# Kernel tuning notes

Hardware: AMD Instinct MI355X
Metric: run time of the kernel (lower is better)

The kernel has to match this reference:

```python
import jax, jax.numpy as jnp
import numpy as np

NHEAD = 3
NPTS = 5
HID = 96
B_GRAPHS = 16384
COORDS_WEIGHT = 1.0


def _ln(x, g, b):
    mu = jnp.mean(x, -1, keepdims=True)
    v = jnp.mean((x - mu) ** 2, -1, keepdims=True)
    return (x - mu) / jnp.sqrt(v + 1e-5) * g + b


def _build_edge_index():
    # fully-connected per graph, grouped by source node (row-major over sources)
    idx = np.arange(NPTS)
    src = np.repeat(idx, NPTS - 1)
    dst = np.concatenate([np.delete(idx, i) for i in range(NPTS)])
    off = (np.arange(B_GRAPHS) * NPTS)[:, None]
    row = (off + src[None, :]).reshape(-1)
    col = (off + dst[None, :]).reshape(-1)
    return jnp.asarray(np.stack([row, col]), dtype=jnp.int32)


def setup_inputs():
    key = jax.random.key(0)
    ks = jax.random.split(key, 24)
    Nn = B_GRAPHS * NPTS          # 81920 nodes
    E = B_GRAPHS * NPTS * (NPTS - 1)  # 327680 edges

    def w(k, i, o):
        return jax.random.normal(k, (i, o), jnp.float32) * (1.0 / np.sqrt(i))

    inp = {
        'h': jax.random.normal(ks[0], (Nn, HID), jnp.float32),
        'edge_index': _build_edge_index(),
        'coord': jax.random.normal(ks[1], (Nn, 3), jnp.float32),
        'coord_pre': jax.random.normal(ks[2], (Nn, 3), jnp.float32),
        'vel': jax.random.normal(ks[3], (Nn, 3), jnp.float32),
        'edge_attr': jax.random.normal(ks[4], (E, HID), jnp.float32),
        # edge_mlp
        'ew1': w(ks[5], 3 * HID, HID), 'eb1': jnp.zeros((HID,), jnp.float32),
        'ew2': w(ks[6], HID, HID), 'eb2': jnp.zeros((HID,), jnp.float32),
        # edge_mlp_enhance
        'xw1': w(ks[7], 3 * HID, HID), 'xb1': jnp.zeros((HID,), jnp.float32),
        'xw2': w(ks[8], HID, HID), 'xb2': jnp.zeros((HID,), jnp.float32),
        # node_mlp
        'nw1': w(ks[9], 2 * HID, HID), 'nb1': jnp.zeros((HID,), jnp.float32),
        'nw2': w(ks[10], HID, HID), 'nb2': jnp.zeros((HID,), jnp.float32),
        # coord_mlp_inner
        'cw1': w(ks[11], HID, HID), 'cb1': jnp.zeros((HID,), jnp.float32),
        'cw2': w(ks[12], HID, HID), 'cb2': jnp.zeros((HID,), jnp.float32),
        'cw3': w(ks[13], HID, 3), 'cb3': jnp.zeros((3,), jnp.float32),
        # attention projections
        'qw': w(ks[14], HID, HID), 'qb': jnp.zeros((HID,), jnp.float32),
        'kw': w(ks[15], 2 * HID, HID), 'kb': jnp.zeros((HID,), jnp.float32),
        'vw': w(ks[16], HID, HID), 'vb': jnp.zeros((HID,), jnp.float32),
        # layernorms
        'g1': jnp.ones((HID,), jnp.float32), 'be1': jnp.zeros((HID,), jnp.float32),
        'g2': jnp.ones((HID,), jnp.float32), 'be2': jnp.zeros((HID,), jnp.float32),
    }
    return inp


def _forward(h, edge_index, coord, coord_pre, vel, edge_attr,
             ew1, eb1, ew2, eb2, xw1, xb1, xw2, xb2, nw1, nb1, nw2, nb2,
             cw1, cb1, cw2, cb2, cw3, cb3, qw, qb, kw, kb, vw, vb,
             g1, be1, g2, be2):
    sp = jax.nn.softplus
    row, col = edge_index[0], edge_index[1]
    n_nodes = h.shape[0]

    # edge_model (attention flag is False)
    ef = sp(jnp.concatenate([h[row], h[col], edge_attr], 1) @ ew1 + eb1)
    ef = sp(ef @ ew2 + eb2)  # [E, C]

    B, N, C = n_nodes // NPTS, NPTS, ef.shape[-1]
    d = C // NHEAD
    q = h.reshape(B, N, C)
    m = ef.reshape(B, N, N - 1, C)
    h_m = jnp.concatenate(
        [jnp.broadcast_to(q[:, :, None, :], (B, N, N - 1, C)), m], -1
    ).reshape(B, N * (N - 1), 2 * C)

    qh = (q @ qw + qb).reshape(B, N, NHEAD, d).transpose(0, 2, 1, 3)           # [B,H,N,d]
    kh = (h_m @ kw + kb).reshape(B, N * (N - 1), NHEAD, d).transpose(0, 2, 1, 3)
    kh = kh.reshape(B, NHEAD, N, N - 1, d)                                      # [B,H,N,N-1,d]
    vh = (ef.reshape(B, N * (N - 1), C) @ vw + vb).reshape(B, N * (N - 1), NHEAD, d).transpose(0, 2, 1, 3)

    scores = jnp.einsum('bhnd,bhnkd->bhnk', qh, kh) / jnp.sqrt(jnp.float32(d))
    attw = jax.nn.softmax(scores, -1)                                           # [B,H,N,N-1]
    m_update = attw.reshape(B, NHEAD, N * (N - 1), 1) * vh                      # [B,H,E',d]
    att_edge_feat = m_update.transpose(0, 2, 1, 3).reshape(-1, C)               # [E, C]

    # node_model
    agg = jax.ops.segment_sum(att_edge_feat, row, num_segments=n_nodes)
    agg = _ln(agg, g1, be1)
    out = sp(jnp.concatenate([h, agg], 1) @ nw1 + nb1) @ nw2 + nb2
    hn = _ln(h + out, g2, be2)

    # edge enhance
    ef2 = ef + (sp(jnp.concatenate([hn[row], hn[col], edge_attr], 1) @ xw1 + xb1) @ xw2 + xb2)

    # coord2radial on coord_pre (norm_diff=False)
    cd = coord_pre[row] - coord_pre[col]
    cc = jnp.cross(coord_pre[row], coord_pre[col])
    cv = jnp.cross(cd, cc)

    # acc_model_inner
    t = sp(ef2 @ cw1 + cb1)
    t = sp(t @ cw2 + cb2)
    bc = t @ cw3 + cb3                                                          # [E, 3]
    trans = jnp.clip(cd * bc[:, :1] + cc * bc[:, 1:2] + cv * bc[:, 2:3], -100.0, 100.0)
    s = jax.ops.segment_sum(trans, row, num_segments=n_nodes)
    cnt = jax.ops.segment_sum(jnp.ones_like(trans), row, num_segments=n_nodes)
    acc = (s / jnp.maximum(cnt, 1.0)) * COORDS_WEIGHT

    return acc, hn, ef2


def reference(h, edge_index, coord, coord_pre, vel, edge_attr,
              ew1, eb1, ew2, eb2, xw1, xb1, xw2, xb2, nw1, nb1, nw2, nb2,
              cw1, cb1, cw2, cb2, cw3, cb3, qw, qb, kw, kb, vw, vb,
              g1, be1, g2, be2):
    return _forward(h, edge_index, coord, coord_pre, vel, edge_attr,
                    ew1, eb1, ew2, eb2, xw1, xb1, xw2, xb2, nw1, nb1, nw2, nb2,
                    cw1, cb1, cw2, cb2, cw3, cb3, qw, qb, kw, kb, vw, vb,
                    g1, be1, g2, be2)
```

## Files before the change

kernel.cpp:

```cpp
#include <hip/hip_runtime.h>
#include <hip/hip_bf16.h>

#define B_GRAPHS 16384
#define NN (B_GRAPHS * 5)
#define NE (NN * 4)
#define GPB 4
#define EPB 80
#define NPB 20

typedef __attribute__((ext_vector_type(8))) short bf8;
typedef __attribute__((ext_vector_type(4))) short s4;
typedef __attribute__((ext_vector_type(4))) float f4;
typedef __attribute__((ext_vector_type(2))) unsigned u2;
typedef __attribute__((ext_vector_type(4))) unsigned u4;

#define OFF_EW1 0
#define OFF_EW2 27648
#define OFF_KW  36864
#define OFF_VW  55296
#define OFF_QW  64512
#define OFF_NW1 73728
#define OFF_NW2 92160
#define OFF_XW1 101376
#define OFF_XW2 129024
#define OFF_CW1 138240
#define OFF_CW2 147456

__device__ __forceinline__ float sp_f(float x) {
    return fmaxf(x, 0.0f) + __logf(1.0f + __expf(-fabsf(x)));
}
__device__ __forceinline__ short tobf(float x) {
    return __builtin_bit_cast(short, __float2bfloat16(x));
}
__device__ __forceinline__ float frombf(short s) {
    union { float f; unsigned u; } v;
    v.u = ((unsigned)(unsigned short)s) << 16;
    return v.f;
}
__device__ __forceinline__ unsigned pk2(float a, float b) {
    unsigned lo = (unsigned short)tobf(a);
    unsigned hi = (unsigned short)tobf(b);
    return lo | (hi << 16);
}
__device__ __forceinline__ bf8 ldfrag(const short* buf, int row, int k) {
    return *(const bf8*)&buf[(row * 96 + k) ^ ((row & 7) << 3)];
}
__device__ __forceinline__ void stpk(short* buf, int row, int col0, f4 v) {
    u2 o = {pk2(v[0], v[1]), pk2(v[2], v[3])};
    *(u2*)&buf[(row * 96 + col0) ^ ((row & 7) << 3)] = o;
}
__device__ __forceinline__ void stpk8(short* buf, int row, int col0,
                                      const float* v) {
    u4 o = {pk2(v[0], v[1]), pk2(v[2], v[3]), pk2(v[4], v[5]), pk2(v[6], v[7])};
    *(u4*)&buf[(row * 96 + col0) ^ ((row & 7) << 3)] = o;
}

template <int K, int NS, class AF>
__device__ __forceinline__ void gemmCol(const short* __restrict__ wT, int wc0,
                                        int ln, int kg, AF aload, f4* acc) {
    constexpr int NK = K / 32;
    bf8 wf[NK];
    const short* wp = wT + (size_t)(wc0 + ln) * K + kg * 8;
#pragma unroll
    for (int kk = 0; kk < NK; kk++) wf[kk] = *(const bf8*)(wp + kk * 32);
#pragma unroll
    for (int s = 0; s < NS; s++) {
        acc[s][0] = 0.f; acc[s][1] = 0.f; acc[s][2] = 0.f; acc[s][3] = 0.f;
    }
#pragma unroll
    for (int kk = 0; kk < NK; kk++) {
#pragma unroll
        for (int s = 0; s < NS; s++) {
            acc[s] = __builtin_amdgcn_mfma_f32_16x16x32_bf16(wf[kk],
                                                             aload(s, kk * 32),
                                                             acc[s], 0, 0, 0);
        }
    }
}

__global__ __launch_bounds__(256) void k_prep(
    const float* ew1, const float* ew2, const float* kw, const float* vw,
    const float* qw, const float* nw1, const float* nw2, const float* xw1,
    const float* xw2, const float* cw1, const float* cw2, short* wsT) {
    const float* srcs[11] = {ew1, ew2, kw, vw, qw, nw1, nw2, xw1, xw2, cw1, cw2};
    const int Ks[11] = {288, 96, 192, 96, 96, 192, 96, 288, 96, 96, 96};
    const int offs[11] = {OFF_EW1, OFF_EW2, OFF_KW, OFF_VW, OFF_QW, OFF_NW1,
                          OFF_NW2, OFF_XW1, OFF_XW2, OFF_CW1, OFF_CW2};
    int b = blockIdx.x;
    const float* src = srcs[b];
    int K = Ks[b], off = offs[b];
    for (int idx = threadIdx.x; idx < K * 96; idx += 256) {
        int n = idx / K, k = idx - n * K;
        wsT[off + idx] = tobf(src[(size_t)k * 96 + n]);
    }
}

__global__ __launch_bounds__(384, 4) void k_fused(
    const float* __restrict__ h, const float* __restrict__ cp,
    const float* __restrict__ ea, const short* __restrict__ wsT,
    const float* __restrict__ eb1, const float* __restrict__ eb2,
    const float* __restrict__ qb, const float* __restrict__ kb,
    const float* __restrict__ vb, const float* __restrict__ nb1,
    const float* __restrict__ nb2, const float* __restrict__ g1,
    const float* __restrict__ be1, const float* __restrict__ g2,
    const float* __restrict__ be2, const float* __restrict__ xb1,
    const float* __restrict__ xb2, const float* __restrict__ cb1,
    const float* __restrict__ cb2, const float* __restrict__ cw3,
    const float* __restrict__ cb3,
    float* __restrict__ accg, float* __restrict__ hng, float* __restrict__ efg) {
    __shared__ __align__(16) short smem[19680];
    short* hb = smem;
    short* SB = smem + 1920;
    short* E1 = smem + 3840;
    short* E2 = smem + 11520;
    float* sc   = (float*)(smem + 19200);
    float* bcb  = sc;
    float* cw3s = (float*)SB;
    float* trs  = (float*)(SB + 640);

    const int t = threadIdx.x;
    const int blk = blockIdx.x;
    const int n0 = blk * NPB, e0 = blk * EPB;

    for (int i = t; i < 1920; i += 384) {
        int r = i / 24, c = (i - r * 24) * 4;
        f4 v = *(const f4*)&ea[(size_t)(e0 + r) * 96 + c];
        stpk(E2, r, c, v);
    }
    for (int i = t; i < 480; i += 384) {
        int r = i / 24, c = (i - r * 24) * 4;
        f4 v = *(const f4*)&h[(size_t)(n0 + r) * 96 + c];
        stpk(hb, r, c, v);
    }
    __syncthreads();

    const int lane = t & 63, w = t >> 6;
    const int kg = lane >> 4, ln = lane & 15;
    const int wc0 = w * 16, col0 = wc0 + kg * 4;

    int erow[5], esrc[5], edst[5];
#pragma unroll
    for (int s = 0; s < 5; s++) {
        erow[s] = s * 16 + ln;
        int sl = erow[s] >> 2;
        esrc[s] = sl;
        int si = sl % 5, jj = erow[s] & 3;
        edst[s] = (sl / 5) * 5 + jj + (jj >= si);
    }

    f4 acc[5];
    gemmCol<288, 5>(wsT + OFF_EW1, wc0, ln, kg,
        [&](int s, int k0) -> bf8 {
            int k = k0 + kg * 8;
            if (k0 < 96)  return ldfrag(hb, esrc[s], k);
            if (k0 < 192) return ldfrag(hb, edst[s], k - 96);
            return ldfrag(E2, erow[s], k - 192);
        }, acc);
    {
        f4 b = *(const f4*)&eb1[col0];
#pragma unroll
        for (int s = 0; s < 5; s++) {
            f4 v;
#pragma unroll
            for (int j = 0; j < 4; j++) v[j] = sp_f(acc[s][j] + b[j]);
            stpk(E1, erow[s], col0, v);
        }
    }
    __syncthreads();
    gemmCol<96, 5>(wsT + OFF_EW2, wc0, ln, kg,
        [&](int s, int k0) { return ldfrag(E1, erow[s], k0 + kg * 8); }, acc);
    {
        f4 qa[2];
        gemmCol<96, 2>(wsT + OFF_QW, wc0, ln, kg,
            [&](int s, int k0) { return ldfrag(hb, s * 16 + ln, k0 + kg * 8); }, qa);
        f4 b = *(const f4*)&eb2[col0];
#pragma unroll
        for (int s = 0; s < 5; s++) {
            f4 v;
#pragma unroll
            for (int j = 0; j < 4; j++) v[j] = sp_f(acc[s][j] + b[j]);
            stpk(E2, erow[s], col0, v);
        }
        f4 bq = *(const f4*)&qb[col0];
#pragma unroll
        for (int s = 0; s < 2; s++) {
            int row = s * 16 + ln;
            if (row < NPB) {
                f4 v;
#pragma unroll
                for (int j = 0; j < 4; j++) v[j] = qa[s][j] + bq[j];
                stpk(SB, row, col0, v);
            }
        }
    }
    __syncthreads();
    gemmCol<192, 5>(wsT + OFF_KW, wc0, ln, kg,
        [&](int s, int k0) {
            int k = k0 + kg * 8;
            if (k0 < 96) return ldfrag(hb, esrc[s], k);
            return ldfrag(E2, erow[s], k - 96);
        }, acc);
    {
        f4 b = *(const f4*)&kb[col0];
#pragma unroll
        for (int s = 0; s < 5; s++) {
            f4 v;
#pragma unroll
            for (int j = 0; j < 4; j++) v[j] = acc[s][j] + b[j];
            stpk(E1, erow[s], col0, v);
        }
    }
    __syncthreads();
    if (t < 240) {
        int e = t / 3, hd = t - e * 3, nd = e >> 2;
        float s = 0.f;
#pragma unroll
        for (int c8 = 0; c8 < 4; c8++) {
            int c = hd * 32 + c8 * 8;
            bf8 qv = ldfrag(SB, nd, c);
            bf8 kv = ldfrag(E1, e, c);
#pragma unroll
            for (int j = 0; j < 8; j++) s = fmaf(frombf(qv[j]), frombf(kv[j]), s);
        }
        sc[e * 3 + hd] = s * 0.17677669529663687f;
    }
    __syncthreads();
    if (t < 60) {
        int nd = t / 3, hd = t - nd * 3;
        float v0 = sc[(nd * 4 + 0) * 3 + hd], v1 = sc[(nd * 4 + 1) * 3 + hd];
        float v2 = sc[(nd * 4 + 2) * 3 + hd], v3 = sc[(nd * 4 + 3) * 3 + hd];
        float m = fmaxf(fmaxf(v0, v1), fmaxf(v2, v3));
        float p0 = __expf(v0 - m), p1 = __expf(v1 - m);
        float p2 = __expf(v2 - m), p3 = __expf(v3 - m);
        float inv = 1.f / (p0 + p1 + p2 + p3);
        sc[(nd * 4 + 0) * 3 + hd] = p0 * inv;
        sc[(nd * 4 + 1) * 3 + hd] = p1 * inv;
        sc[(nd * 4 + 2) * 3 + hd] = p2 * inv;
        sc[(nd * 4 + 3) * 3 + hd] = p3 * inv;
    }
    gemmCol<96, 5>(wsT + OFF_VW, wc0, ln, kg,
        [&](int s, int k0) { return ldfrag(E2, erow[s], k0 + kg * 8); }, acc);
    {
        f4 b = *(const f4*)&vb[col0];
#pragma unroll
        for (int s = 0; s < 5; s++) {
            f4 v;
#pragma unroll
            for (int j = 0; j < 4; j++) v[j] = acc[s][j] + b[j];
            stpk(E1, erow[s], col0, v);
        }
    }
    __syncthreads();
    if (t < 320) {
        int nd = t >> 4, cg = t & 15;
        bool act = cg < 12;
        int hd = cg >> 2;
        float agg[8];
#pragma unroll
        for (int j = 0; j < 8; j++) agg[j] = 0.f;
        if (act) {
#pragma unroll
            for (int k = 0; k < 4; k++) {
                int e = nd * 4 + k;
                float wgt = sc[e * 3 + hd];
                bf8 v8 = ldfrag(E1, e, cg * 8);
#pragma unroll
                for (int j = 0; j < 8; j++) agg[j] = fmaf(wgt, frombf(v8[j]), agg[j]);
            }
        }
        float s1 = 0.f, s2 = 0.f;
#pragma unroll
        for (int j = 0; j < 8; j++) { s1 += agg[j]; s2 += agg[j] * agg[j]; }
        if (!act) { s1 = 0.f; s2 = 0.f; }
        for (int m = 1; m < 16; m <<= 1) {
            s1 += __shfl_xor(s1, m);
            s2 += __shfl_xor(s2, m);
        }
        float mu = s1 * (1.f / 96.f);
        float var = s2 * (1.f / 96.f) - mu * mu;
        float rs = rsqrtf(var + 1e-5f);
        if (act) {
            int c = cg * 8;
            f4 ga = *(const f4*)&g1[c], gb = *(const f4*)&g1[c + 4];
            f4 ba = *(const f4*)&be1[c], bb = *(const f4*)&be1[c + 4];
            float o[8];
#pragma unroll
            for (int j = 0; j < 4; j++) {
                o[j] = (agg[j] - mu) * rs * ga[j] + ba[j];
                o[j + 4] = (agg[j + 4] - mu) * rs * gb[j] + bb[j];
            }
            stpk8(SB, nd, c, o);
        }
    }
    __syncthreads();
    {
        f4 eav[5];
        int rr[5], cc[5];
#pragma unroll
        for (int u = 0; u < 5; u++) {
            int i = t + u * 384;
            rr[u] = i / 24; cc[u] = (i - rr[u] * 24) * 4;
            eav[u] = *(const f4*)&ea[(size_t)(e0 + rr[u]) * 96 + cc[u]];
        }
        f4 na[2];
        gemmCol<192, 2>(wsT + OFF_NW1, wc0, ln, kg,
            [&](int s, int k0) {
                int row = s * 16 + ln, k = k0 + kg * 8;
                if (k0 < 96) return ldfrag(hb, row, k);
                return ldfrag(SB, row, k - 96);
            }, na);
        f4 b = *(const f4*)&nb1[col0];
        f4 t1v[2];
#pragma unroll
        for (int s = 0; s < 2; s++)
#pragma unroll
            for (int j = 0; j < 4; j++) t1v[s][j] = sp_f(na[s][j] + b[j]);
        __syncthreads();
#pragma unroll
        for (int s = 0; s < 2; s++) {
            int row = s * 16 + ln;
            if (row < NPB) stpk(SB, row, col0, t1v[s]);
        }
#pragma unroll
        for (int u = 0; u < 5; u++) stpk(E1, rr[u], cc[u], eav[u]);
    }
    __syncthreads();
    {
        f4 na[2];
        gemmCol<96, 2>(wsT + OFF_NW2, wc0, ln, kg,
            [&](int s, int k0) { return ldfrag(SB, s * 16 + ln, k0 + kg * 8); }, na);
        f4 b = *(const f4*)&nb2[col0];
#pragma unroll
        for (int s = 0; s < 2; s++) {
            int row = s * 16 + ln;
            if (row < NPB) {
                f4 hv = *(const f4*)&h[(size_t)(n0 + row) * 96 + col0];
                f4 v;
#pragma unroll
                for (int j = 0; j < 4; j++) v[j] = na[s][j] + b[j] + hv[j];
                stpk(hb, row, col0, v);
            }
        }
    }
    __syncthreads();
    if (t < 320) {
        int nd = t >> 4, cg = t & 15;
        bool act = cg < 12;
        float xv[8];
#pragma unroll
        for (int j = 0; j < 8; j++) xv[j] = 0.f;
        if (act) {
            bf8 x = ldfrag(hb, nd, cg * 8);
#pragma unroll
            for (int j = 0; j < 8; j++) xv[j] = frombf(x[j]);
        }
        float s1 = 0.f, s2 = 0.f;
#pragma unroll
        for (int j = 0; j < 8; j++) { s1 += xv[j]; s2 += xv[j] * xv[j]; }
        for (int m = 1; m < 16; m <<= 1) {
            s1 += __shfl_xor(s1, m);
            s2 += __shfl_xor(s2, m);
        }
        float mu = s1 * (1.f / 96.f);
        float var = s2 * (1.f / 96.f) - mu * mu;
        float rs = rsqrtf(var + 1e-5f);
        if (act) {
            int c = cg * 8;
            f4 ga = *(const f4*)&g2[c], gb = *(const f4*)&g2[c + 4];
            f4 ba = *(const f4*)&be2[c], bb = *(const f4*)&be2[c + 4];
            float o[8];
#pragma unroll
            for (int j = 0; j < 4; j++) {
                o[j] = (xv[j] - mu) * rs * ga[j] + ba[j];
                o[j + 4] = (xv[j + 4] - mu) * rs * gb[j] + bb[j];
            }
            f4 o0 = {o[0], o[1], o[2], o[3]}, o1 = {o[4], o[5], o[6], o[7]};
            *(f4*)&hng[(size_t)(n0 + nd) * 96 + c] = o0;
            *(f4*)&hng[(size_t)(n0 + nd) * 96 + c + 4] = o1;
            stpk8(hb, nd, c, o);
        }
    }
    __syncthreads();
    gemmCol<288, 5>(wsT + OFF_XW1, wc0, ln, kg,
        [&](int s, int k0) -> bf8 {
            int k = k0 + kg * 8;
            if (k0 < 96)  return ldfrag(hb, esrc[s], k);
            if (k0 < 192) return ldfrag(hb, edst[s], k - 96);
            return ldfrag(E1, erow[s], k - 192);
        }, acc);
    __syncthreads();
    {
        f4 b = *(const f4*)&xb1[col0];
#pragma unroll
        for (int s = 0; s < 5; s++) {
            f4 v;
#pragma unroll
            for (int j = 0; j < 4; j++) v[j] = sp_f(acc[s][j] + b[j]);
            stpk(E1, erow[s], col0, v);
        }
    }
    __syncthreads();
    gemmCol<96, 5>(wsT + OFF_XW2, wc0, ln, kg,
        [&](int s, int k0) { return ldfrag(E1, erow[s], k0 + kg * 8); }, acc);
    {
        f4 b = *(const f4*)&xb2[col0];
#pragma unroll
        for (int s = 0; s < 5; s++) {
            int row = erow[s];
            s4 ev = *(const s4*)&E2[(row * 96 + col0) ^ ((row & 7) << 3)];
            f4 v;
#pragma unroll
            for (int j = 0; j < 4; j++) v[j] = acc[s][j] + b[j] + frombf(ev[j]);
            *(f4*)&efg[(size_t)(e0 + row) * 96 + col0] = v;
            stpk(E2, row, col0, v);
        }
    }
    __syncthreads();
    gemmCol<96, 5>(wsT + OFF_CW1, wc0, ln, kg,
        [&](int s, int k0) { return ldfrag(E2, erow[s], k0 + kg * 8); }, acc);
    {
        f4 b = *(const f4*)&cb1[col0];
#pragma unroll
        for (int s = 0; s < 5; s++) {
            f4 v;
#pragma unroll
            for (int j = 0; j < 4; j++) v[j] = sp_f(acc[s][j] + b[j]);
            stpk(E1, erow[s], col0, v);
        }
    }
    __syncthreads();
    if (t < 288) cw3s[t] = cw3[t];
    gemmCol<96, 5>(wsT + OFF_CW2, wc0, ln, kg,
        [&](int s, int k0) { return ldfrag(E1, erow[s], k0 + kg * 8); }, acc);
    {
        f4 b = *(const f4*)&cb2[col0];
#pragma unroll
        for (int s = 0; s < 5; s++) {
            f4 v;
#pragma unroll
            for (int j = 0; j < 4; j++) v[j] = sp_f(acc[s][j] + b[j]);
            stpk(E2, erow[s], col0, v);
        }
    }
    __syncthreads();
    if (t < 240) {
        int e = t / 3, j = t - e * 3;
        float s = cb3[j];
#pragma unroll
        for (int c8 = 0; c8 < 12; c8++) {
            bf8 av = ldfrag(E2, e, c8 * 8);
#pragma unroll
            for (int jj = 0; jj < 8; jj++)
                s = fmaf(frombf(av[jj]), cw3s[(c8 * 8 + jj) * 3 + j], s);
        }
        bcb[e * 3 + j] = s;
    }
    __syncthreads();
    if (t < 80) {
        int sl = t >> 2, jj = t & 3, si = sl % 5;
        int dl = (sl / 5) * 5 + jj + (jj >= si);
        int rn = n0 + sl, cn = n0 + dl;
        float r0c = cp[(size_t)rn * 3 + 0], r1c = cp[(size_t)rn * 3 + 1],
              r2c = cp[(size_t)rn * 3 + 2];
        float q0 = cp[(size_t)cn * 3 + 0], q1 = cp[(size_t)cn * 3 + 1],
              q2 = cp[(size_t)cn * 3 + 2];
        float d0 = r0c - q0, d1 = r1c - q1, d2 = r2c - q2;
        float x0 = r1c * q2 - r2c * q1;
        float x1 = r2c * q0 - r0c * q2;
        float x2 = r0c * q1 - r1c * q0;
        float v0 = d1 * x2 - d2 * x1;
        float v1 = d2 * x0 - d0 * x2;
        float v2 = d0 * x1 - d1 * x0;
        float b0 = bcb[t * 3 + 0], b1 = bcb[t * 3 + 1], b2 = bcb[t * 3 + 2];
        trs[t * 4 + 0] = fminf(fmaxf(d0 * b0 + x0 * b1 + v0 * b2, -100.f), 100.f);
        trs[t * 4 + 1] = fminf(fmaxf(d1 * b0 + x1 * b1 + v1 * b2, -100.f), 100.f);
        trs[t * 4 + 2] = fminf(fmaxf(d2 * b0 + x2 * b1 + v2 * b2, -100.f), 100.f);
    }
    __syncthreads();
    if (t < 60) {
        int nd = t / 3, j = t - nd * 3;
        float s = (trs[(nd * 4 + 0) * 4 + j] + trs[(nd * 4 + 1) * 4 + j] +
                   trs[(nd * 4 + 2) * 4 + j] + trs[(nd * 4 + 3) * 4 + j]) * 0.25f;
        accg[(size_t)(n0 + nd) * 3 + j] = s;
    }
}

extern "C" void kernel_launch(void* const* d_in, const int* in_sizes, int n_in,
                              void* d_out, int out_size, void* d_ws, size_t ws_size,
                              hipStream_t stream) {
    const float* h   = (const float*)d_in[0];
    const float* cp  = (const float*)d_in[3];
    const float* ea  = (const float*)d_in[5];
    const float* ew1 = (const float*)d_in[6];
    const float* eb1 = (const float*)d_in[7];
    const float* ew2 = (const float*)d_in[8];
    const float* eb2 = (const float*)d_in[9];
    const float* xw1 = (const float*)d_in[10];
    const float* xb1 = (const float*)d_in[11];
    const float* xw2 = (const float*)d_in[12];
    const float* xb2 = (const float*)d_in[13];
    const float* nw1 = (const float*)d_in[14];
    const float* nb1 = (const float*)d_in[15];
    const float* nw2 = (const float*)d_in[16];
    const float* nb2 = (const float*)d_in[17];
    const float* cw1 = (const float*)d_in[18];
    const float* cb1 = (const float*)d_in[19];
    const float* cw2 = (const float*)d_in[20];
    const float* cb2 = (const float*)d_in[21];
    const float* cw3 = (const float*)d_in[22];
    const float* cb3 = (const float*)d_in[23];
    const float* qw  = (const float*)d_in[24];
    const float* qb  = (const float*)d_in[25];
    const float* kw  = (const float*)d_in[26];
    const float* kb  = (const float*)d_in[27];
    const float* vw  = (const float*)d_in[28];
    const float* vb  = (const float*)d_in[29];
    const float* g1  = (const float*)d_in[30];
    const float* be1 = (const float*)d_in[31];
    const float* g2  = (const float*)d_in[32];
    const float* be2 = (const float*)d_in[33];

    float* out  = (float*)d_out;
    float* accg = out;
    float* hng  = out + (size_t)NN * 3;
    float* efg  = out + (size_t)NN * 3 + (size_t)NN * 96;
    short* wsT = (short*)d_ws;

    k_prep<<<11, 256, 0, stream>>>(ew1, ew2, kw, vw, qw, nw1, nw2, xw1, xw2,
                                   cw1, cw2, wsT);
    k_fused<<<B_GRAPHS / GPB, 384, 0, stream>>>(
        h, cp, ea, wsT, eb1, eb2, qb, kb, vb, nb1, nb2, g1, be1, g2, be2,
        xb1, xb2, cb1, cb2, cw3, cb3, accg, hng, efg);
}
```

Before: 393.6 us.

## Double graphs per block to amortize weight fragment loads over more edges

Each block now processes 8 graphs (160 edges, 40 nodes) instead of 4, so every MFMA column pass reuses each loaded weight fragment across 10 row tiles instead of 5. Shared memory doubles, occupancy drops from 4 to 3 blocks per CU, and the node and small per-edge phases become strided loops. It also swaps which buffers (hb/SB) hold node-MLP intermediates so the larger node tiles fit. The cost is higher register pressure from doubled accumulators and fewer resident waves to hide latency.

```diff
diff --git a/kernel.cpp b/kernel.cpp
--- a/kernel.cpp
+++ b/kernel.cpp
@@ -4,9 +4,11 @@
 #define B_GRAPHS 16384
 #define NN (B_GRAPHS * 5)
 #define NE (NN * 4)
-#define GPB 4
-#define EPB 80
-#define NPB 20
+#define GPB 8
+#define EPB 160
+#define NPB 40
+#define EST 10
+#define NST 3
 
 typedef __attribute__((ext_vector_type(8))) short bf8;
 typedef __attribute__((ext_vector_type(4))) short s4;
@@ -95,7 +97,7 @@
     }
 }
 
-__global__ __launch_bounds__(384, 4) void k_fused(
+__global__ __launch_bounds__(384, 3) void k_fused(
     const float* __restrict__ h, const float* __restrict__ cp,
     const float* __restrict__ ea, const short* __restrict__ wsT,
     const float* __restrict__ eb1, const float* __restrict__ eb2,
@@ -108,12 +110,12 @@
     const float* __restrict__ cb2, const float* __restrict__ cw3,
     const float* __restrict__ cb3,
     float* __restrict__ accg, float* __restrict__ hng, float* __restrict__ efg) {
-    __shared__ __align__(16) short smem[19680];
+    __shared__ __align__(16) short smem[39360];
     short* hb = smem;
-    short* SB = smem + 1920;
-    short* E1 = smem + 3840;
-    short* E2 = smem + 11520;
-    float* sc   = (float*)(smem + 19200);
+    short* SB = smem + 3840;
+    short* E1 = smem + 7680;
+    short* E2 = smem + 23040;
+    float* sc   = (float*)(smem + 38400);
     float* bcb  = sc;
     float* cw3s = (float*)SB;
     float* trs  = (float*)(SB + 640);
@@ -122,12 +124,12 @@
     const int blk = blockIdx.x;
     const int n0 = blk * NPB, e0 = blk * EPB;
 
-    for (int i = t; i < 1920; i += 384) {
+    for (int i = t; i < EPB * 24; i += 384) {
         int r = i / 24, c = (i - r * 24) * 4;
         f4 v = *(const f4*)&ea[(size_t)(e0 + r) * 96 + c];
         stpk(E2, r, c, v);
     }
-    for (int i = t; i < 480; i += 384) {
+    for (int i = t; i < NPB * 24; i += 384) {
         int r = i / 24, c = (i - r * 24) * 4;
         f4 v = *(const f4*)&h[(size_t)(n0 + r) * 96 + c];
         stpk(hb, r, c, v);
@@ -138,52 +140,52 @@
     const int kg = lane >> 4, ln = lane & 15;
     const int wc0 = w * 16, col0 = wc0 + kg * 4;
 
-    int erow[5], esrc[5], edst[5];
-#pragma unroll
-    for (int s = 0; s < 5; s++) {
-        erow[s] = s * 16 + ln;
-        int sl = erow[s] >> 2;
+    int esrc[EST], edst[EST];
+#pragma unroll
+    for (int s = 0; s < EST; s++) {
+        int er = s * 16 + ln;
+        int sl = er >> 2;
         esrc[s] = sl;
-        int si = sl % 5, jj = erow[s] & 3;
+        int si = sl % 5, jj = ln & 3;
         edst[s] = (sl / 5) * 5 + jj + (jj >= si);
     }
 
-    f4 acc[5];
-    gemmCol<288, 5>(wsT + OFF_EW1, wc0, ln, kg,
+    f4 acc[EST];
+    gemmCol<288, EST>(wsT + OFF_EW1, wc0, ln, kg,
         [&](int s, int k0) -> bf8 {
             int k = k0 + kg * 8;
             if (k0 < 96)  return ldfrag(hb, esrc[s], k);
             if (k0 < 192) return ldfrag(hb, edst[s], k - 96);
-            return ldfrag(E2, erow[s], k - 192);
+            return ldfrag(E2, s * 16 + ln, k - 192);
         }, acc);
     {
         f4 b = *(const f4*)&eb1[col0];
 #pragma unroll
-        for (int s = 0; s < 5; s++) {
+        for (int s = 0; s < EST; s++) {
             f4 v;
 #pragma unroll
             for (int j = 0; j < 4; j++) v[j] = sp_f(acc[s][j] + b[j]);
-            stpk(E1, erow[s], col0, v);
-        }
-    }
-    __syncthreads();
-    gemmCol<96, 5>(wsT + OFF_EW2, wc0, ln, kg,
-        [&](int s, int k0) { return ldfrag(E1, erow[s], k0 + kg * 8); }, acc);
-    {
-        f4 qa[2];
-        gemmCol<96, 2>(wsT + OFF_QW, wc0, ln, kg,
+            stpk(E1, s * 16 + ln, col0, v);
+        }
+    }
+    __syncthreads();
+    gemmCol<96, EST>(wsT + OFF_EW2, wc0, ln, kg,
+        [&](int s, int k0) { return ldfrag(E1, s * 16 + ln, k0 + kg * 8); }, acc);
+    {
+        f4 qa[NST];
+        gemmCol<96, NST>(wsT + OFF_QW, wc0, ln, kg,
             [&](int s, int k0) { return ldfrag(hb, s * 16 + ln, k0 + kg * 8); }, qa);
         f4 b = *(const f4*)&eb2[col0];
 #pragma unroll
-        for (int s = 0; s < 5; s++) {
+        for (int s = 0; s < EST; s++) {
             f4 v;
 #pragma unroll
             for (int j = 0; j < 4; j++) v[j] = sp_f(acc[s][j] + b[j]);
-            stpk(E2, erow[s], col0, v);
+            stpk(E2, s * 16 + ln, col0, v);
         }
         f4 bq = *(const f4*)&qb[col0];
 #pragma unroll
-        for (int s = 0; s < 2; s++) {
+        for (int s = 0; s < NST; s++) {
             int row = s * 16 + ln;
             if (row < NPB) {
                 f4 v;
@@ -194,25 +196,25 @@
         }
     }
     __syncthreads();
-    gemmCol<192, 5>(wsT + OFF_KW, wc0, ln, kg,
+    gemmCol<192, EST>(wsT + OFF_KW, wc0, ln, kg,
         [&](int s, int k0) {
             int k = k0 + kg * 8;
             if (k0 < 96) return ldfrag(hb, esrc[s], k);
-            return ldfrag(E2, erow[s], k - 96);
+            return ldfrag(E2, s * 16 + ln, k - 96);
         }, acc);
     {
         f4 b = *(const f4*)&kb[col0];
 #pragma unroll
-        for (int s = 0; s < 5; s++) {
+        for (int s = 0; s < EST; s++) {
             f4 v;
 #pragma unroll
             for (int j = 0; j < 4; j++) v[j] = acc[s][j] + b[j];
-            stpk(E1, erow[s], col0, v);
-        }
-    }
-    __syncthreads();
-    if (t < 240) {
-        int e = t / 3, hd = t - e * 3, nd = e >> 2;
+            stpk(E1, s * 16 + ln, col0, v);
+        }
+    }
+    __syncthreads();
+    for (int i = t; i < EPB * 3; i += 384) {
+        int e = i / 3, hd = i - e * 3, nd = e >> 2;
         float s = 0.f;
 #pragma unroll
         for (int c8 = 0; c8 < 4; c8++) {
@@ -225,7 +227,7 @@
         sc[e * 3 + hd] = s * 0.17677669529663687f;
     }
     __syncthreads();
-    if (t < 60) {
+    if (t < NPB * 3) {
         int nd = t / 3, hd = t - nd * 3;
         float v0 = sc[(nd * 4 + 0) * 3 + hd], v1 = sc[(nd * 4 + 1) * 3 + hd];
         float v2 = sc[(nd * 4 + 2) * 3 + hd], v3 = sc[(nd * 4 + 3) * 3 + hd];
@@ -238,175 +240,180 @@
         sc[(nd * 4 + 2) * 3 + hd] = p2 * inv;
         sc[(nd * 4 + 3) * 3 + hd] = p3 * inv;
     }
-    gemmCol<96, 5>(wsT + OFF_VW, wc0, ln, kg,
-        [&](int s, int k0) { return ldfrag(E2, erow[s], k0 + kg * 8); }, acc);
+    gemmCol<96, EST>(wsT + OFF_VW, wc0, ln, kg,
+        [&](int s, int k0) { return ldfrag(E2, s * 16 + ln, k0 + kg * 8); }, acc);
     {
         f4 b = *(const f4*)&vb[col0];
 #pragma unroll
-        for (int s = 0; s < 5; s++) {
+        for (int s = 0; s < EST; s++) {
             f4 v;
 #pragma unroll
             for (int j = 0; j < 4; j++) v[j] = acc[s][j] + b[j];
-            stpk(E1, erow[s], col0, v);
-        }
-    }
-    __syncthreads();
-    if (t < 320) {
-        int nd = t >> 4, cg = t & 15;
+            stpk(E1, s * 16 + ln, col0, v);
+        }
+    }
+    __syncthreads();
+    {
+        int grp = t >> 4, cg = t & 15;
         bool act = cg < 12;
         int hd = cg >> 2;
-        float agg[8];
-#pragma unroll
-        for (int j = 0; j < 8; j++) agg[j] = 0.f;
-        if (act) {
-#pragma unroll
-            for (int k = 0; k < 4; k++) {
-                int e = nd * 4 + k;
-                float wgt = sc[e * 3 + hd];
-                bf8 v8 = ldfrag(E1, e, cg * 8);
-#pragma unroll
-                for (int j = 0; j < 8; j++) agg[j] = fmaf(wgt, frombf(v8[j]), agg[j]);
-            }
-        }
-        float s1 = 0.f, s2 = 0.f;
-#pragma unroll
-        for (int j = 0; j < 8; j++) { s1 += agg[j]; s2 += agg[j] * agg[j]; }
-        if (!act) { s1 = 0.f; s2 = 0.f; }
-        for (int m = 1; m < 16; m <<= 1) {
-            s1 += __shfl_xor(s1, m);
-            s2 += __shfl_xor(s2, m);
-        }
-        float mu = s1 * (1.f / 96.f);
-        float var = s2 * (1.f / 96.f) - mu * mu;
-        float rs = rsqrtf(var + 1e-5f);
-        if (act) {
-            int c = cg * 8;
-            f4 ga = *(const f4*)&g1[c], gb = *(const f4*)&g1[c + 4];
-            f4 ba = *(const f4*)&be1[c], bb = *(const f4*)&be1[c + 4];
-            float o[8];
-#pragma unroll
-            for (int j = 0; j < 4; j++) {
-                o[j] = (agg[j] - mu) * rs * ga[j] + ba[j];
-                o[j + 4] = (agg[j + 4] - mu) * rs * gb[j] + bb[j];
-            }
-            stpk8(SB, nd, c, o);
-        }
-    }
-    __syncthreads();
-    {
-        f4 eav[5];
-        int rr[5], cc[5];
-#pragma unroll
-        for (int u = 0; u < 5; u++) {
+        for (int nd = grp; nd < NPB; nd += 24) {
+            float agg[8];
+#pragma unroll
+            for (int j = 0; j < 8; j++) agg[j] = 0.f;
+            if (act) {
+#pragma unroll
+                for (int k = 0; k < 4; k++) {
+                    int e = nd * 4 + k;
+                    float wgt = sc[e * 3 + hd];
+                    bf8 v8 = ldfrag(E1, e, cg * 8);
+#pragma unroll
+                    for (int j = 0; j < 8; j++)
+                        agg[j] = fmaf(wgt, frombf(v8[j]), agg[j]);
+                }
+            }
+            float s1 = 0.f, s2 = 0.f;
+#pragma unroll
+            for (int j = 0; j < 8; j++) { s1 += agg[j]; s2 += agg[j] * agg[j]; }
+            if (!act) { s1 = 0.f; s2 = 0.f; }
+            for (int m = 1; m < 16; m <<= 1) {
+                s1 += __shfl_xor(s1, m);
+                s2 += __shfl_xor(s2, m);
+            }
+            float mu = s1 * (1.f / 96.f);
+            float var = s2 * (1.f / 96.f) - mu * mu;
+            float rs = rsqrtf(var + 1e-5f);
+            if (act) {
+                int c = cg * 8;
+                f4 ga = *(const f4*)&g1[c], gb = *(const f4*)&g1[c + 4];
+                f4 ba = *(const f4*)&be1[c], bb = *(const f4*)&be1[c + 4];
+                float o[8];
+#pragma unroll
+                for (int j = 0; j < 4; j++) {
+                    o[j] = (agg[j] - mu) * rs * ga[j] + ba[j];
+                    o[j + 4] = (agg[j + 4] - mu) * rs * gb[j] + bb[j];
+                }
+                stpk8(SB, nd, c, o);
+            }
+        }
+    }
+    __syncthreads();
+    {
+        f4 eav[10];
+        int rr[10], cc[10];
+#pragma unroll
+        for (int u = 0; u < 10; u++) {
             int i = t + u * 384;
             rr[u] = i / 24; cc[u] = (i - rr[u] * 24) * 4;
             eav[u] = *(const f4*)&ea[(size_t)(e0 + rr[u]) * 96 + cc[u]];
         }
-        f4 na[2];
-        gemmCol<192, 2>(wsT + OFF_NW1, wc0, ln, kg,
+        f4 na[NST];
+        gemmCol<192, NST>(wsT + OFF_NW1, wc0, ln, kg,
             [&](int s, int k0) {
                 int row = s * 16 + ln, k = k0 + kg * 8;
                 if (k0 < 96) return ldfrag(hb, row, k);
                 return ldfrag(SB, row, k - 96);
             }, na);
         f4 b = *(const f4*)&nb1[col0];
-        f4 t1v[2];
-#pragma unroll
-        for (int s = 0; s < 2; s++)
+        f4 t1v[NST];
+#pragma unroll
+        for (int s = 0; s < NST; s++)
 #pragma unroll
             for (int j = 0; j < 4; j++) t1v[s][j] = sp_f(na[s][j] + b[j]);
         __syncthreads();
 #pragma unroll
-        for (int s = 0; s < 2; s++) {
+        for (int s = 0; s < NST; s++) {
             int row = s * 16 + ln;
-            if (row < NPB) stpk(SB, row, col0, t1v[s]);
-        }
-#pragma unroll
-        for (int u = 0; u < 5; u++) stpk(E1, rr[u], cc[u], eav[u]);
-    }
-    __syncthreads();
-    {
-        f4 na[2];
-        gemmCol<96, 2>(wsT + OFF_NW2, wc0, ln, kg,
-            [&](int s, int k0) { return ldfrag(SB, s * 16 + ln, k0 + kg * 8); }, na);
+            if (row < NPB) stpk(hb, row, col0, t1v[s]);
+        }
+#pragma unroll
+        for (int u = 0; u < 10; u++) stpk(E1, rr[u], cc[u], eav[u]);
+    }
+    __syncthreads();
+    {
+        f4 na[NST];
+        gemmCol<96, NST>(wsT + OFF_NW2, wc0, ln, kg,
+            [&](int s, int k0) { return ldfrag(hb, s * 16 + ln, k0 + kg * 8); }, na);
         f4 b = *(const f4*)&nb2[col0];
 #pragma unroll
-        for (int s = 0; s < 2; s++) {
+        for (int s = 0; s < NST; s++) {
             int row = s * 16 + ln;
             if (row < NPB) {
                 f4 hv = *(const f4*)&h[(size_t)(n0 + row) * 96 + col0];
                 f4 v;
 #pragma unroll
                 for (int j = 0; j < 4; j++) v[j] = na[s][j] + b[j] + hv[j];
-                stpk(hb, row, col0, v);
-            }
-        }
-    }
-    __syncthreads();
-    if (t < 320) {
-        int nd = t >> 4, cg = t & 15;
+                stpk(SB, row, col0, v);
+            }
+        }
+    }
+    __syncthreads();
+    {
+        int grp = t >> 4, cg = t & 15;
         bool act = cg < 12;
-        float xv[8];
-#pragma unroll
-        for (int j = 0; j < 8; j++) xv[j] = 0.f;
-        if (act) {
-            bf8 x = ldfrag(hb, nd, cg * 8);
-#pragma unroll
-            for (int j = 0; j < 8; j++) xv[j] = frombf(x[j]);
-        }
-        float s1 = 0.f, s2 = 0.f;
-#pragma unroll
-        for (int j = 0; j < 8; j++) { s1 += xv[j]; s2 += xv[j] * xv[j]; }
-        for (int m = 1; m < 16; m <<= 1) {
-            s1 += __shfl_xor(s1, m);
-            s2 += __shfl_xor(s2, m);
-        }
-        float mu = s1 * (1.f / 96.f);
-        float var = s2 * (1.f / 96.f) - mu * mu;
-        float rs = rsqrtf(var + 1e-5f);
-        if (act) {
-            int c = cg * 8;
-            f4 ga = *(const f4*)&g2[c], gb = *(const f4*)&g2[c + 4];
-            f4 ba = *(const f4*)&be2[c], bb = *(const f4*)&be2[c + 4];
-            float o[8];
-#pragma unroll
-            for (int j = 0; j < 4; j++) {
-                o[j] = (xv[j] - mu) * rs * ga[j] + ba[j];
-                o[j + 4] = (xv[j + 4] - mu) * rs * gb[j] + bb[j];
-            }
-            f4 o0 = {o[0], o[1], o[2], o[3]}, o1 = {o[4], o[5], o[6], o[7]};
-            *(f4*)&hng[(size_t)(n0 + nd) * 96 + c] = o0;
-            *(f4*)&hng[(size_t)(n0 + nd) * 96 + c + 4] = o1;
-            stpk8(hb, nd, c, o);
-        }
-    }
-    __syncthreads();
-    gemmCol<288, 5>(wsT + OFF_XW1, wc0, ln, kg,
+        for (int nd = grp; nd < NPB; nd += 24) {
+            float xv[8];
+#pragma unroll
+            for (int j = 0; j < 8; j++) xv[j] = 0.f;
+            if (act) {
+                bf8 x = ldfrag(SB, nd, cg * 8);
+#pragma unroll
+                for (int j = 0; j < 8; j++) xv[j] = frombf(x[j]);
+            }
+            float s1 = 0.f, s2 = 0.f;
+#pragma unroll
+            for (int j = 0; j < 8; j++) { s1 += xv[j]; s2 += xv[j] * xv[j]; }
+            for (int m = 1; m < 16; m <<= 1) {
+                s1 += __shfl_xor(s1, m);
+                s2 += __shfl_xor(s2, m);
+            }
+            float mu = s1 * (1.f / 96.f);
+            float var = s2 * (1.f / 96.f) - mu * mu;
+            float rs = rsqrtf(var + 1e-5f);
+            if (act) {
+                int c = cg * 8;
+                f4 ga = *(const f4*)&g2[c], gb = *(const f4*)&g2[c + 4];
+                f4 ba = *(const f4*)&be2[c], bb = *(const f4*)&be2[c + 4];
+                float o[8];
+#pragma unroll
+                for (int j = 0; j < 4; j++) {
+                    o[j] = (xv[j] - mu) * rs * ga[j] + ba[j];
+                    o[j + 4] = (xv[j + 4] - mu) * rs * gb[j] + bb[j];
+                }
+                f4 o0 = {o[0], o[1], o[2], o[3]}, o1 = {o[4], o[5], o[6], o[7]};
+                *(f4*)&hng[(size_t)(n0 + nd) * 96 + c] = o0;
+                *(f4*)&hng[(size_t)(n0 + nd) * 96 + c + 4] = o1;
+                stpk8(hb, nd, c, o);
+            }
+        }
+    }
+    __syncthreads();
+    gemmCol<288, EST>(wsT + OFF_XW1, wc0, ln, kg,
         [&](int s, int k0) -> bf8 {
             int k = k0 + kg * 8;
             if (k0 < 96)  return ldfrag(hb, esrc[s], k);
             if (k0 < 192) return ldfrag(hb, edst[s], k - 96);
-            return ldfrag(E1, erow[s], k - 192);
+            return ldfrag(E1, s * 16 + ln, k - 192);
         }, acc);
     __syncthreads();
     {
         f4 b = *(const f4*)&xb1[col0];
 #pragma unroll
-        for (int s = 0; s < 5; s++) {
+        for (int s = 0; s < EST; s++) {
             f4 v;
 #pragma unroll
             for (int j = 0; j < 4; j++) v[j] = sp_f(acc[s][j] + b[j]);
-            stpk(E1, erow[s], col0, v);
-        }
-    }
-    __syncthreads();
-    gemmCol<96, 5>(wsT + OFF_XW2, wc0, ln, kg,
-        [&](int s, int k0) { return ldfrag(E1, erow[s], k0 + kg * 8); }, acc);
+            stpk(E1, s * 16 + ln, col0, v);
+        }
+    }
+    __syncthreads();
+    gemmCol<96, EST>(wsT + OFF_XW2, wc0, ln, kg,
+        [&](int s, int k0) { return ldfrag(E1, s * 16 + ln, k0 + kg * 8); }, acc);
     {
         f4 b = *(const f4*)&xb2[col0];
 #pragma unroll
-        for (int s = 0; s < 5; s++) {
-            int row = erow[s];
+        for (int s = 0; s < EST; s++) {
+            int row = s * 16 + ln;
             s4 ev = *(const s4*)&E2[(row * 96 + col0) ^ ((row & 7) << 3)];
             f4 v;
 #pragma unroll
@@ -416,35 +423,35 @@
         }
     }
     __syncthreads();
-    gemmCol<96, 5>(wsT + OFF_CW1, wc0, ln, kg,
-        [&](int s, int k0) { return ldfrag(E2, erow[s], k0 + kg * 8); }, acc);
+    gemmCol<96, EST>(wsT + OFF_CW1, wc0, ln, kg,
+        [&](int s, int k0) { return ldfrag(E2, s * 16 + ln, k0 + kg * 8); }, acc);
     {
         f4 b = *(const f4*)&cb1[col0];
 #pragma unroll
-        for (int s = 0; s < 5; s++) {
+        for (int s = 0; s < EST; s++) {
             f4 v;
 #pragma unroll
             for (int j = 0; j < 4; j++) v[j] = sp_f(acc[s][j] + b[j]);
-            stpk(E1, erow[s], col0, v);
+            stpk(E1, s * 16 + ln, col0, v);
         }
     }
     __syncthreads();
     if (t < 288) cw3s[t] = cw3[t];
-    gemmCol<96, 5>(wsT + OFF_CW2, wc0, ln, kg,
-        [&](int s, int k0) { return ldfrag(E1, erow[s], k0 + kg * 8); }, acc);
+    gemmCol<96, EST>(wsT + OFF_CW2, wc0, ln, kg,
+        [&](int s, int k0) { return ldfrag(E1, s * 16 + ln, k0 + kg * 8); }, acc);
     {
         f4 b = *(const f4*)&cb2[col0];
 #pragma unroll
-        for (int s = 0; s < 5; s++) {
+        for (int s = 0; s < EST; s++) {
             f4 v;
 #pragma unroll
             for (int j = 0; j < 4; j++) v[j] = sp_f(acc[s][j] + b[j]);
-            stpk(E2, erow[s], col0, v);
-        }
-    }
-    __syncthreads();
-    if (t < 240) {
-        int e = t / 3, j = t - e * 3;
+            stpk(E2, s * 16 + ln, col0, v);
+        }
+    }
+    __syncthreads();
+    for (int i = t; i < EPB * 3; i += 384) {
+        int e = i / 3, j = i - e * 3;
         float s = cb3[j];
 #pragma unroll
         for (int c8 = 0; c8 < 12; c8++) {
@@ -456,7 +463,7 @@
         bcb[e * 3 + j] = s;
     }
     __syncthreads();
-    if (t < 80) {
+    if (t < EPB) {
         int sl = t >> 2, jj = t & 3, si = sl % 5;
         int dl = (sl / 5) * 5 + jj + (jj >= si);
         int rn = n0 + sl, cn = n0 + dl;
@@ -477,7 +484,7 @@
         trs[t * 4 + 2] = fminf(fmaxf(d2 * b0 + x2 * b1 + v2 * b2, -100.f), 100.f);
     }
     __syncthreads();
-    if (t < 60) {
+    if (t < NPB * 3) {
         int nd = t / 3, j = t - nd * 3;
         float s = (trs[(nd * 4 + 0) * 4 + j] + trs[(nd * 4 + 1) * 4 + j] +
                    trs[(nd * 4 + 2) * 4 + j] + trs[(nd * 4 + 3) * 4 + j]) * 0.25f;
```

Measured after the change: 591.4 us. +50.2%, slower.
